# Kernel optimization log

Hardware: AMD Instinct MI355X
Metric: run time of the kernel (lower is better)

## Reference

```python
import jax, jax.numpy as jnp
import numpy as np

N_NODES = 50000
N_EDGES = 600000
D = 128
DROP_P = 0.5


def setup_inputs() -> dict:
    key = jax.random.key(0)
    k1, k2, k3, k4, k5, k6 = jax.random.split(key, 6)
    x = jax.random.normal(k1, (N_NODES, D), dtype=jnp.float32)
    W = jax.random.normal(k2, (D, D), dtype=jnp.float32) * (1.0 / np.sqrt(D))
    b = jax.random.normal(k3, (D,), dtype=jnp.float32) * 0.01
    mask_u = jax.random.uniform(k4, (N_NODES, D), dtype=jnp.float32)
    src = jax.random.randint(k5, (N_EDGES,), 0, N_NODES, dtype=jnp.int64)
    dst = jax.random.randint(k6, (N_EDGES,), 0, N_NODES, dtype=jnp.int64)
    return {"x": x, "W": W, "b": b, "mask_u": mask_u, "src": src, "dst": dst}


def reference(x, W, b, mask_u, src, dst):
    n_nodes = x.shape[0]
    # linear + relu (nn.Linear stores weight as [out, in]; here W is [out, in])
    h = jax.nn.relu(jnp.einsum('nd,od->no', x, W) + b)
    # inverted dropout with precomputed uniform noise (train mode, p=0.5)
    keep = (mask_u >= DROP_P).astype(h.dtype)
    h = h * keep * (1.0 / (1.0 - DROP_P))
    # message passing: msg = h[src], reduce = sum over incoming edges per dst
    msgs = jnp.take(h, src, axis=0)            # [E, D] gather
    out = jax.ops.segment_sum(msgs, dst, num_segments=n_nodes)  # [N, D]
    return out
```

## Files before the change

### kernel.cpp

```cpp
#include <hip/hip_runtime.h>

#define D 128
#define TILE_N 16
#define HPITCH 132
#define RNODES 256
#define FCAP 48
#define LCAP 32
#define SPILL_MAX 8192

typedef __attribute__((ext_vector_type(8))) short  short8;
typedef __attribute__((ext_vector_type(4))) float  f32x4;

__device__ inline unsigned short f32_to_bf16(float f) {
    unsigned int u = __float_as_uint(f);
    unsigned int r = (u + 0x7FFFu + ((u >> 16) & 1u)) >> 16;
    return (unsigned short)r;
}
__device__ inline float bf16_to_f32(unsigned short s) {
    return __uint_as_float(((unsigned int)s) << 16);
}
__device__ inline short8 pack_bf16x8(float4 a, float4 b) {
    short8 u;
    u[0] = (short)f32_to_bf16(a.x); u[1] = (short)f32_to_bf16(a.y);
    u[2] = (short)f32_to_bf16(a.z); u[3] = (short)f32_to_bf16(a.w);
    u[4] = (short)f32_to_bf16(b.x); u[5] = (short)f32_to_bf16(b.y);
    u[6] = (short)f32_to_bf16(b.z); u[7] = (short)f32_to_bf16(b.w);
    return u;
}

__global__ __launch_bounds__(256) void zero_kernel(int* __restrict__ p, int n)
{
    int i = blockIdx.x * 256 + threadIdx.x;
    if (i < n) p[i] = 0;
}

__global__ __launch_bounds__(256) void prepbin_kernel(
    const float* __restrict__ W, unsigned short* __restrict__ Wb,
    const float* __restrict__ mask_u, unsigned char* __restrict__ mbits,
    int n_nodes,
    const int* __restrict__ src, const int* __restrict__ dst,
    int n_edges, int chunk, int n_ranges,
    unsigned int* __restrict__ seg, int* __restrict__ cnt_grid,
    int* __restrict__ spill_cnt, int* __restrict__ spill)
{
    __shared__ __align__(16) char smem[50176];
    const int t = threadIdx.x;

    if ((int)blockIdx.x < n_ranges) {
        int* s_fcnt = (int*)smem;
        unsigned int* s_fifo = (unsigned int*)(smem + 1024);
        const int b  = blockIdx.x;
        const int nb = n_ranges;

        for (int i = t; i < n_ranges; i += 256) s_fcnt[i] = 0;
        __syncthreads();

        const int e0 = b * chunk;
        const int e1 = (e0 + chunk < n_edges) ? e0 + chunk : n_edges;
        for (int i = e0 + t; i < e1; i += 256) {
            int dd = dst[i];
            int ss = src[i];
            int r  = dd >> 8;
            int pos = atomicAdd(&s_fcnt[r], 1);
            if (pos < FCAP) {
                s_fifo[r * FCAP + pos] = ((unsigned)dd << 16) | (unsigned)ss;
            } else {
                int k = atomicAdd(spill_cnt, 1);
                if (k < SPILL_MAX) { spill[2 * k] = dd; spill[2 * k + 1] = ss; }
            }
        }
        __syncthreads();

        for (int f = t; f < n_ranges * FCAP; f += 256) {
            int r = f / FCAP, slot = f - r * FCAP;
            if (slot < s_fcnt[r])
                seg[((size_t)r * nb + b) * FCAP + slot] = s_fifo[f];
        }
        for (int r = t; r < n_ranges; r += 256) {
            int c = s_fcnt[r];
            cnt_grid[r * nb + b] = (c > FCAP) ? FCAP : c;
        }
    } else {
        const int bid = blockIdx.x - n_ranges;
        const int nconv = gridDim.x - n_ranges;
        const int tid = bid * 256 + t;
        const int nth = nconv * 256;

        for (int i = tid; i < (D * D) / 8; i += nth) {
            float4 v0 = *(const float4*)&W[i * 8];
            float4 v1 = *(const float4*)&W[i * 8 + 4];
            *(short8*)&Wb[i * 8] = pack_bf16x8(v0, v1);
        }
        const int nx8 = n_nodes * (D / 8);
        for (int i = tid; i < nx8; i += nth) {
            float4 m0 = *(const float4*)&mask_u[(size_t)i * 8];
            float4 m1 = *(const float4*)&mask_u[(size_t)i * 8 + 4];
            unsigned b = 0;
            b |= (m0.x >= 0.5f) ? 1u : 0u;   b |= (m0.y >= 0.5f) ? 2u : 0u;
            b |= (m0.z >= 0.5f) ? 4u : 0u;   b |= (m0.w >= 0.5f) ? 8u : 0u;
            b |= (m1.x >= 0.5f) ? 16u : 0u;  b |= (m1.y >= 0.5f) ? 32u : 0u;
            b |= (m1.z >= 0.5f) ? 64u : 0u;  b |= (m1.w >= 0.5f) ? 128u : 0u;
            mbits[i] = (unsigned char)b;
        }
    }
}

__global__ __launch_bounds__(256, 8) void mega_kernel(
    const float* __restrict__ x, const unsigned short* __restrict__ Wb,
    const float* __restrict__ bias, const unsigned char* __restrict__ mbits,
    unsigned short* __restrict__ h, int n_nodes,
    const unsigned int* __restrict__ seg, const int* __restrict__ cnt_grid,
    int nb1, int n_ranges,
    int* __restrict__ deg, unsigned short* __restrict__ bucket,
    int* __restrict__ spill_cnt, int* __restrict__ spill)
{
    __shared__ __align__(16) char smem[19712];
    const int t = threadIdx.x;

    if ((int)blockIdx.x < n_ranges) {
        int* s_pref = (int*)smem;
        int* s_cnt  = (int*)(smem + 1024);
        int* s_ncnt = (int*)(smem + 2048);
        unsigned short* s_slots = (unsigned short*)(smem + 3072);
        const int r = blockIdx.x;
        const unsigned rbase = (unsigned)r << 8;

        int v = (t < nb1) ? cnt_grid[r * nb1 + t] : 0;
        s_pref[t] = v;
        s_cnt[t]  = v;
        s_ncnt[t] = 0;
        __syncthreads();
        for (int o = 1; o < 256; o <<= 1) {
            int add = (t >= o) ? s_pref[t - o] : 0;
            __syncthreads();
            s_pref[t] += add;
            __syncthreads();
        }
        const int total = s_pref[255];

        for (int f = t; f < total; f += 256) {
            int lo = 0, hi = nb1 - 1;
            while (lo < hi) {
                int mid = (lo + hi) >> 1;
                if (s_pref[mid] > f) hi = mid; else lo = mid + 1;
            }
            int slot = f - (s_pref[lo] - s_cnt[lo]);
            unsigned pk = seg[((size_t)r * nb1 + lo) * FCAP + slot];
            unsigned dd = pk >> 16;
            unsigned ss = pk & 0xFFFFu;
            int rel = (int)(dd - rbase);
            int pos = atomicAdd(&s_ncnt[rel], 1);
            if (pos < LCAP) {
                s_slots[(rel << 5) + pos] = (unsigned short)ss;
            } else {
                int k = atomicAdd(spill_cnt, 1);
                if (k < SPILL_MAX) { spill[2 * k] = (int)dd; spill[2 * k + 1] = (int)ss; }
            }
        }
        __syncthreads();

        const int node = (int)rbase + t;
        if (node < n_nodes) {
            int c = s_ncnt[t];
            deg[node] = (c > LCAP) ? LCAP : c;
        }
        for (int vv = t; vv < 1024; vv += 256) {
            int rel = vv >> 2;
            int gn  = (int)rbase + rel;
            if (gn < n_nodes)
                *(short8*)&bucket[((size_t)gn << 5) + ((vv & 3) << 3)] =
                    *(const short8*)&s_slots[vv << 3];
        }
    } else {
        unsigned short* ht = (unsigned short*)smem;
        const int lane = t & 63;
        const int w    = t >> 6;
        const int fr   = lane & 15;
        const int fg   = lane >> 4;
        const int n0 = (blockIdx.x - n_ranges) * TILE_N;

        const int prow = t >> 4;
        const int pcg  = t & 15;
        const int pnode = n0 + prow;
        const bool pvalid = (pnode < n_nodes);
        unsigned mbyte = 0;
        if (pvalid) mbyte = mbits[pnode * 16 + pcg];

        int arow = n0 + fr;
        if (arow >= n_nodes) arow = n_nodes - 1;
        const float* xr = x + (size_t)arow * D;
        short8 a0 = pack_bf16x8(*(const float4*)&xr[ 0 + fg * 8],
                                *(const float4*)&xr[ 4 + fg * 8]);
        short8 a1 = pack_bf16x8(*(const float4*)&xr[32 + fg * 8],
                                *(const float4*)&xr[36 + fg * 8]);
        short8 a2 = pack_bf16x8(*(const float4*)&xr[64 + fg * 8],
                                *(const float4*)&xr[68 + fg * 8]);
        short8 a3 = pack_bf16x8(*(const float4*)&xr[96 + fg * 8],
                                *(const float4*)&xr[100 + fg * 8]);

        const float bs0 = bias[32 * w + fr];
        const float bs1 = bias[32 * w + 16 + fr];
        const unsigned short* wb0 = Wb + (size_t)(32 * w + fr) * D;
        const unsigned short* wb1 = Wb + (size_t)(32 * w + 16 + fr) * D;

        f32x4 acc0 = (f32x4){0.f, 0.f, 0.f, 0.f};
        f32x4 acc1 = (f32x4){0.f, 0.f, 0.f, 0.f};
        #pragma unroll
        for (int s = 0; s < 4; ++s) {
            short8 a = (s == 0) ? a0 : (s == 1) ? a1 : (s == 2) ? a2 : a3;
            short8 b0 = *(const short8*)&wb0[s * 32 + fg * 8];
            short8 b1 = *(const short8*)&wb1[s * 32 + fg * 8];
            acc0 = __builtin_amdgcn_mfma_f32_16x16x32_bf16(a, b0, acc0, 0, 0, 0);
            acc1 = __builtin_amdgcn_mfma_f32_16x16x32_bf16(a, b1, acc1, 0, 0, 0);
        }

        #pragma unroll
        for (int rr = 0; rr < 4; ++rr) {
            const int rl = fg * 4 + rr;
            float v0 = fmaxf(acc0[rr] + bs0, 0.f);
            float v1 = fmaxf(acc1[rr] + bs1, 0.f);
            ht[rl * HPITCH + 32 * w + fr]      = f32_to_bf16(v0);
            ht[rl * HPITCH + 32 * w + 16 + fr] = f32_to_bf16(v1);
        }
        __syncthreads();

        if (pvalid) {
            short8 hv = *(const short8*)&ht[prow * HPITCH + pcg * 8];
            short8 o;
            #pragma unroll
            for (int j = 0; j < 8; ++j) {
                float v = bf16_to_f32((unsigned short)hv[j]) * 2.f;
                o[j] = ((mbyte >> j) & 1u) ? (short)f32_to_bf16(v) : (short)0;
            }
            *(short8*)&h[(size_t)pnode * D + pcg * 8] = o;
        }
    }
}

__global__ __launch_bounds__(256) void gather_reduce_kernel(
    const unsigned short* __restrict__ h, const int* __restrict__ deg,
    const unsigned short* __restrict__ bucket, float* __restrict__ out,
    int n_nodes)
{
    const int t = threadIdx.x;
    const int node = blockIdx.x * 16 + (t >> 4);
    if (node >= n_nodes) return;
    const int cb = (t & 15) * 8;
    int dg = deg[node];
    if (dg > LCAP) dg = LCAP;
    const unsigned short* b = bucket + ((size_t)node << 5);

    float acc[8];
    #pragma unroll
    for (int j = 0; j < 8; ++j) acc[j] = 0.f;

    int i = 0;
    for (; i + 3 < dg; i += 4) {
        int s0 = b[i], s1 = b[i + 1], s2 = b[i + 2], s3 = b[i + 3];
        short8 v0 = *(const short8*)&h[(size_t)s0 * D + cb];
        short8 v1 = *(const short8*)&h[(size_t)s1 * D + cb];
        short8 v2 = *(const short8*)&h[(size_t)s2 * D + cb];
        short8 v3 = *(const short8*)&h[(size_t)s3 * D + cb];
        #pragma unroll
        for (int j = 0; j < 8; ++j)
            acc[j] += (bf16_to_f32((unsigned short)v0[j]) +
                       bf16_to_f32((unsigned short)v1[j])) +
                      (bf16_to_f32((unsigned short)v2[j]) +
                       bf16_to_f32((unsigned short)v3[j]));
    }
    for (; i < dg; ++i) {
        int s0 = b[i];
        short8 v0 = *(const short8*)&h[(size_t)s0 * D + cb];
        #pragma unroll
        for (int j = 0; j < 8; ++j) acc[j] += bf16_to_f32((unsigned short)v0[j]);
    }

    f32x4 o0 = (f32x4){acc[0], acc[1], acc[2], acc[3]};
    f32x4 o1 = (f32x4){acc[4], acc[5], acc[6], acc[7]};
    __builtin_nontemporal_store(o0, (f32x4*)&out[(size_t)node * D + cb]);
    __builtin_nontemporal_store(o1, (f32x4*)&out[(size_t)node * D + cb + 4]);
}

__global__ __launch_bounds__(256) void spill_apply_kernel(
    const unsigned short* __restrict__ h, const int* __restrict__ spill_cnt,
    const int* __restrict__ spill, float* __restrict__ out)
{
    int n = *spill_cnt;
    if (n > SPILL_MAX) n = SPILL_MAX;
    for (int e = (int)(threadIdx.x >> 4); e < n; e += 16) {
        int dd = spill[2 * e], ss = spill[2 * e + 1];
        int cb = (threadIdx.x & 15) * 8;
        short8 v = *(const short8*)&h[(size_t)ss * D + cb];
        float* o = &out[(size_t)dd * D + cb];
        #pragma unroll
        for (int j = 0; j < 8; ++j)
            atomicAdd(o + j, bf16_to_f32((unsigned short)v[j]));
    }
}

__global__ __launch_bounds__(256) void gemm_fb_kernel(
    const float* __restrict__ x, const float* __restrict__ W,
    const float* __restrict__ bias, const float* __restrict__ mask_u,
    unsigned short* __restrict__ h, int n_nodes)
{
    int tid = blockIdx.x * 256 + threadIdx.x;
    if (tid >= n_nodes * 16) return;
    int node = tid >> 4, cg = tid & 15;
    for (int c = 0; c < 8; ++c) {
        int col = cg * 8 + c;
        float s = bias[col];
        for (int k = 0; k < D; ++k)
            s += bf16_to_f32(f32_to_bf16(x[(size_t)node * D + k])) *
                 bf16_to_f32(f32_to_bf16(W[(size_t)col * D + k]));
        s = fmaxf(s, 0.f);
        float m = mask_u[(size_t)node * D + col];
        s *= (m >= 0.5f) ? 2.f : 0.f;
        h[(size_t)node * D + col] = f32_to_bf16(s);
    }
}

__global__ __launch_bounds__(256) void scatter_atomic_kernel(
    const unsigned short* __restrict__ h, const int* __restrict__ src,
    const int* __restrict__ dst, float* __restrict__ out, int n_edges)
{
    const int t = threadIdx.x;
    const int e = blockIdx.x * 16 + (t >> 4);
    if (e >= n_edges) return;
    const int cb = (t & 15) * 8;
    const int s  = src[e];
    const int dd = dst[e];
    short8 v = *(const short8*)&h[(size_t)s * D + cb];
    float* o = &out[(size_t)dd * D + cb];
    #pragma unroll
    for (int j = 0; j < 8; ++j) atomicAdd(o + j, bf16_to_f32((unsigned short)v[j]));
}

extern "C" void kernel_launch(void* const* d_in, const int* in_sizes, int n_in,
                              void* d_out, int out_size, void* d_ws, size_t ws_size,
                              hipStream_t stream) {
    const float* x      = (const float*)d_in[0];
    const float* W      = (const float*)d_in[1];
    const float* bias   = (const float*)d_in[2];
    const float* mask_u = (const float*)d_in[3];
    const int*   src    = (const int*)d_in[4];
    const int*   dst    = (const int*)d_in[5];
    float* out = (float*)d_out;

    const int n_nodes  = in_sizes[0] / D;
    const int n_edges  = in_sizes[4];
    const int n_tiles  = (n_nodes + TILE_N - 1) / TILE_N;
    const int n_ranges = (n_nodes + RNODES - 1) / RNODES;
    const int nb1      = n_ranges;
    const int chunk    = (n_edges + nb1 - 1) / nb1;

    const size_t wb_bytes = (size_t)D * D * sizeof(unsigned short);
    const size_t h_bytes  = (size_t)n_nodes * D * sizeof(unsigned short);
    char* p = (char*)d_ws;
    unsigned short* Wb = (unsigned short*)p;     p += wb_bytes;
    unsigned short* h  = (unsigned short*)p;     p += h_bytes;
    int* deg       = (int*)p;                    p += (size_t)((n_nodes + 3) & ~3) * sizeof(int);
    int* spill_cnt = (int*)p;                    p += 16;
    int* spill     = (int*)p;                    p += (size_t)2 * SPILL_MAX * sizeof(int);
    unsigned short* bucket = (unsigned short*)p; p += (size_t)n_nodes * LCAP * sizeof(unsigned short);
    unsigned int* seg      = (unsigned int*)p;   p += (size_t)n_ranges * nb1 * FCAP * sizeof(unsigned int);
    int* cnt_grid  = (int*)p;                    p += (size_t)n_ranges * nb1 * sizeof(int);
    unsigned char* mbits = (unsigned char*)p;    p += (size_t)n_nodes * 16;
    const size_t needed = (size_t)(p - (char*)d_ws);

    if (ws_size >= needed && n_nodes <= 65535) {
        zero_kernel<<<1, 256, 0, stream>>>(spill_cnt, 4);
        prepbin_kernel<<<n_ranges + 1024, 256, 0, stream>>>(
            W, Wb, mask_u, mbits, n_nodes,
            src, dst, n_edges, chunk, n_ranges, seg, cnt_grid, spill_cnt, spill);
        mega_kernel<<<n_ranges + n_tiles, 256, 0, stream>>>(
            x, Wb, bias, mbits, h, n_nodes,
            seg, cnt_grid, nb1, n_ranges, deg, bucket, spill_cnt, spill);
        gather_reduce_kernel<<<(n_nodes + 15) / 16, 256, 0, stream>>>(
            h, deg, bucket, out, n_nodes);
        spill_apply_kernel<<<1, 256, 0, stream>>>(h, spill_cnt, spill, out);
    } else {
        unsigned short* hf = (unsigned short*)d_ws;
        gemm_fb_kernel<<<(n_nodes * 16 + 255) / 256, 256, 0, stream>>>(
            x, W, bias, mask_u, hf, n_nodes);
        zero_kernel<<<(out_size + 255) / 256, 256, 0, stream>>>((int*)d_out, out_size);
        scatter_atomic_kernel<<<(n_edges + 15) / 16, 256, 0, stream>>>(
            hf, src, dst, out, n_edges);
    }
}
```

Measured before the change: 76.59 us.

## Read dropout mask directly in GEMM and fold spill edges into gather

Drops the separate mask-to-bitmask pass from the prep kernel. The GEMM epilogue now reads mask_u floats directly, which removes one full read of mask_u plus the bitmask write and read. The separate single-block spill_apply kernel is removed, and each gather thread instead scans the spill list for its node. That scan costs little when nothing spills but becomes quadratic in work if many edges spill. The prep kernel grid shrinks to n_ranges+64 blocks, since only the W conversion is left in its second branch.

After: 76.04 us. No clear change (-0.7%).

```diff
diff --git a/kernel.cpp b/kernel.cpp
--- a/kernel.cpp
+++ b/kernel.cpp
@@ -36,8 +36,6 @@
 
 __global__ __launch_bounds__(256) void prepbin_kernel(
     const float* __restrict__ W, unsigned short* __restrict__ Wb,
-    const float* __restrict__ mask_u, unsigned char* __restrict__ mbits,
-    int n_nodes,
     const int* __restrict__ src, const int* __restrict__ dst,
     int n_edges, int chunk, int n_ranges,
     unsigned int* __restrict__ seg, int* __restrict__ cnt_grid,
@@ -82,32 +80,18 @@
         }
     } else {
         const int bid = blockIdx.x - n_ranges;
-        const int nconv = gridDim.x - n_ranges;
         const int tid = bid * 256 + t;
-        const int nth = nconv * 256;
-
-        for (int i = tid; i < (D * D) / 8; i += nth) {
-            float4 v0 = *(const float4*)&W[i * 8];
-            float4 v1 = *(const float4*)&W[i * 8 + 4];
-            *(short8*)&Wb[i * 8] = pack_bf16x8(v0, v1);
-        }
-        const int nx8 = n_nodes * (D / 8);
-        for (int i = tid; i < nx8; i += nth) {
-            float4 m0 = *(const float4*)&mask_u[(size_t)i * 8];
-            float4 m1 = *(const float4*)&mask_u[(size_t)i * 8 + 4];
-            unsigned b = 0;
-            b |= (m0.x >= 0.5f) ? 1u : 0u;   b |= (m0.y >= 0.5f) ? 2u : 0u;
-            b |= (m0.z >= 0.5f) ? 4u : 0u;   b |= (m0.w >= 0.5f) ? 8u : 0u;
-            b |= (m1.x >= 0.5f) ? 16u : 0u;  b |= (m1.y >= 0.5f) ? 32u : 0u;
-            b |= (m1.z >= 0.5f) ? 64u : 0u;  b |= (m1.w >= 0.5f) ? 128u : 0u;
-            mbits[i] = (unsigned char)b;
+        if (tid < (D * D) / 8) {
+            float4 v0 = *(const float4*)&W[tid * 8];
+            float4 v1 = *(const float4*)&W[tid * 8 + 4];
+            *(short8*)&Wb[tid * 8] = pack_bf16x8(v0, v1);
         }
     }
 }
 
 __global__ __launch_bounds__(256, 8) void mega_kernel(
     const float* __restrict__ x, const unsigned short* __restrict__ Wb,
-    const float* __restrict__ bias, const unsigned char* __restrict__ mbits,
+    const float* __restrict__ bias, const float* __restrict__ mask_u,
     unsigned short* __restrict__ h, int n_nodes,
     const unsigned int* __restrict__ seg, const int* __restrict__ cnt_grid,
     int nb1, int n_ranges,
@@ -183,8 +167,10 @@
         const int pcg  = t & 15;
         const int pnode = n0 + prow;
         const bool pvalid = (pnode < n_nodes);
-        unsigned mbyte = 0;
-        if (pvalid) mbyte = mbits[pnode * 16 + pcg];
+        const int mnode = pvalid ? pnode : (n_nodes - 1);
+        const size_t moff = (size_t)mnode * D + pcg * 8;
+        float4 m0 = *(const float4*)&mask_u[moff];
+        float4 m1 = *(const float4*)&mask_u[moff + 4];
 
         int arow = n0 + fr;
         if (arow >= n_nodes) arow = n_nodes - 1;
@@ -229,8 +215,9 @@
             short8 o;
             #pragma unroll
             for (int j = 0; j < 8; ++j) {
+                float m = (j < 4) ? ((const float*)&m0)[j] : ((const float*)&m1)[j - 4];
                 float v = bf16_to_f32((unsigned short)hv[j]) * 2.f;
-                o[j] = ((mbyte >> j) & 1u) ? (short)f32_to_bf16(v) : (short)0;
+                o[j] = (m >= 0.5f) ? (short)f32_to_bf16(v) : (short)0;
             }
             *(short8*)&h[(size_t)pnode * D + pcg * 8] = o;
         }
@@ -240,7 +227,7 @@
 __global__ __launch_bounds__(256) void gather_reduce_kernel(
     const unsigned short* __restrict__ h, const int* __restrict__ deg,
     const unsigned short* __restrict__ bucket, float* __restrict__ out,
-    int n_nodes)
+    int n_nodes, const int* __restrict__ spill_cnt, const int* __restrict__ spill)
 {
     const int t = threadIdx.x;
     const int node = blockIdx.x * 16 + (t >> 4);
@@ -275,27 +262,24 @@
         for (int j = 0; j < 8; ++j) acc[j] += bf16_to_f32((unsigned short)v0[j]);
     }
 
+    int nsp = *spill_cnt;
+    if (nsp > 0) {
+        if (nsp > SPILL_MAX) nsp = SPILL_MAX;
+        for (int e = 0; e < nsp; ++e) {
+            if (spill[2 * e] == node) {
+                int ss = spill[2 * e + 1];
+                short8 v = *(const short8*)&h[(size_t)ss * D + cb];
+                #pragma unroll
+                for (int j = 0; j < 8; ++j)
+                    acc[j] += bf16_to_f32((unsigned short)v[j]);
+            }
+        }
+    }
+
     f32x4 o0 = (f32x4){acc[0], acc[1], acc[2], acc[3]};
     f32x4 o1 = (f32x4){acc[4], acc[5], acc[6], acc[7]};
     __builtin_nontemporal_store(o0, (f32x4*)&out[(size_t)node * D + cb]);
     __builtin_nontemporal_store(o1, (f32x4*)&out[(size_t)node * D + cb + 4]);
-}
-
-__global__ __launch_bounds__(256) void spill_apply_kernel(
-    const unsigned short* __restrict__ h, const int* __restrict__ spill_cnt,
-    const int* __restrict__ spill, float* __restrict__ out)
-{
-    int n = *spill_cnt;
-    if (n > SPILL_MAX) n = SPILL_MAX;
-    for (int e = (int)(threadIdx.x >> 4); e < n; e += 16) {
-        int dd = spill[2 * e], ss = spill[2 * e + 1];
-        int cb = (threadIdx.x & 15) * 8;
-        short8 v = *(const short8*)&h[(size_t)ss * D + cb];
-        float* o = &out[(size_t)dd * D + cb];
-        #pragma unroll
-        for (int j = 0; j < 8; ++j)
-            atomicAdd(o + j, bf16_to_f32((unsigned short)v[j]));
-    }
 }
 
 __global__ __launch_bounds__(256) void gemm_fb_kernel(
@@ -364,20 +348,18 @@
     unsigned short* bucket = (unsigned short*)p; p += (size_t)n_nodes * LCAP * sizeof(unsigned short);
     unsigned int* seg      = (unsigned int*)p;   p += (size_t)n_ranges * nb1 * FCAP * sizeof(unsigned int);
     int* cnt_grid  = (int*)p;                    p += (size_t)n_ranges * nb1 * sizeof(int);
-    unsigned char* mbits = (unsigned char*)p;    p += (size_t)n_nodes * 16;
     const size_t needed = (size_t)(p - (char*)d_ws);
 
     if (ws_size >= needed && n_nodes <= 65535) {
         zero_kernel<<<1, 256, 0, stream>>>(spill_cnt, 4);
-        prepbin_kernel<<<n_ranges + 1024, 256, 0, stream>>>(
-            W, Wb, mask_u, mbits, n_nodes,
-            src, dst, n_edges, chunk, n_ranges, seg, cnt_grid, spill_cnt, spill);
+        prepbin_kernel<<<n_ranges + 64, 256, 0, stream>>>(
+            W, Wb, src, dst, n_edges, chunk, n_ranges,
+            seg, cnt_grid, spill_cnt, spill);
         mega_kernel<<<n_ranges + n_tiles, 256, 0, stream>>>(
-            x, Wb, bias, mbits, h, n_nodes,
+            x, Wb, bias, mask_u, h, n_nodes,
             seg, cnt_grid, nb1, n_ranges, deg, bucket, spill_cnt, spill);
         gather_reduce_kernel<<<(n_nodes + 15) / 16, 256, 0, stream>>>(
-            h, deg, bucket, out, n_nodes);
-        spill_apply_kernel<<<1, 256, 0, stream>>>(h, spill_cnt, spill, out);
+            h, deg, bucket, out, n_nodes, spill_cnt, spill);
     } else {
         unsigned short* hf = (unsigned short*)d_ws;
         gemm_fb_kernel<<<(n_nodes * 16 + 255) / 256, 256, 0, stream>>>(
```
